# Optimization experiments

Hardware: AMD Instinct MI355X
Metric: run time of the kernel (lower is better)

The kernel has to match this reference:

```python
import jax, jax.numpy as jnp
import numpy as np

BS, T, E, H, CU = 8, 1024, 512, 8, 6
HD = E // H
W_SCALE = 0.05  # keep pre-softmax logits in a sane range


def setup_inputs() -> dict:
    key = jax.random.key(0)
    ks = jax.random.split(key, 9)
    return {
        "x": jax.random.normal(ks[0], (BS, T, E), jnp.float32),
        "u": jax.random.normal(ks[1], (BS, CU, T, T), jnp.float32),
        "umask": jnp.zeros((BS, T, T, 1), jnp.bool_),
        "wq": jax.random.normal(ks[2], (E, E), jnp.float32) * W_SCALE,
        "wk": jax.random.normal(ks[3], (E, E), jnp.float32) * W_SCALE,
        "wv": jax.random.normal(ks[4], (E, E), jnp.float32) * W_SCALE,
        "wo": jax.random.normal(ks[5], (E, E), jnp.float32) * W_SCALE,
        "bo": jnp.zeros((E,), jnp.float32),
        "wu": jax.random.normal(ks[6], (H, CU), jnp.float32) * W_SCALE,
        "bu": jnp.zeros((H,), jnp.float32),
    }


def reference(x, u, umask, wq, wk, wv, wo, bo, wu, bu):
    bs, t, e = x.shape
    h, hd = H, HD
    scaling = hd ** (-0.5)

    # linear projections (torch Linear: y = x @ W^T), split heads -> [b, h, t, hd]
    def proj(w):
        return jnp.einsum('bte,fe->btf', x, w).reshape(bs, t, h, hd).transpose(0, 2, 1, 3)

    Q, K, V = proj(wq), proj(wk), proj(wv)

    # NOTE: faithful to source, which DIVIDES by head_dim**-0.5
    scores = jnp.einsum('bhqd,bhkd->bhqk', Q, K) / scaling

    # 1x1 conv bias projection: [b, cu, t, t] -> [b, h, t, t]
    ubias = jnp.einsum('bcij,hc->bhij', u, wu) + bu[None, :, None, None]
    # umask: [b, t, t, 1] -> swap dims 1 and 3 -> [b, 1, t, t]
    mask_t = jnp.transpose(umask, (0, 3, 2, 1))
    ubias = jnp.where(mask_t, -jnp.inf, ubias)
    scores = scores + ubias

    attn = jax.nn.softmax(scores, axis=-1)
    # dropout p=0.0 -> identity
    ctx = jnp.einsum('bhqk,bhkd->bqhd', attn, V).reshape(bs, t, e)
    out = jnp.einsum('bte,fe->btf', ctx, wo) + bo
    return (out, attn)
```

## Files before the change

### kernel.cpp

```cpp
#include <hip/hip_runtime.h>
#include <cmath>

#define BSZ 8
#define TT  1024
#define EE  512
#define HH  8
#define CUc 6
#define HDD 64

typedef __bf16 bf16;
typedef __attribute__((ext_vector_type(4))) float f32x4;
typedef __attribute__((ext_vector_type(8))) float f32x8;
typedef __attribute__((ext_vector_type(4))) bf16  bf16x4;
typedef __attribute__((ext_vector_type(8))) bf16  bf16x8;

static __device__ __forceinline__ f32x4 mfma16(bf16x8 a, bf16x8 b, f32x4 c) {
    return __builtin_amdgcn_mfma_f32_16x16x32_bf16(a, b, c, 0, 0, 0);
}
static __device__ __forceinline__ void glds16(const bf16* g, bf16* l) {
    __builtin_amdgcn_global_load_lds((const __attribute__((address_space(1))) void*)g,
                                     (__attribute__((address_space(3))) void*)l, 16, 0, 0);
}

__global__ __launch_bounds__(256) void k_split_all(
    const float* __restrict__ wq, const float* __restrict__ wk,
    const float* __restrict__ wv, const float* __restrict__ wo,
    bf16* __restrict__ wqh, bf16* __restrict__ wql,
    bf16* __restrict__ wkh, bf16* __restrict__ wkl,
    bf16* __restrict__ wvh, bf16* __restrict__ woh)
{
    const float* src; bf16* hi; bf16* lo;
    switch (blockIdx.y) {
        case 0: src = wq; hi = wqh; lo = wql;     break;
        case 1: src = wk; hi = wkh; lo = wkl;     break;
        case 2: src = wv; hi = wvh; lo = nullptr; break;
        default: src = wo; hi = woh; lo = nullptr; break;
    }
    const int i = (blockIdx.x * 256 + threadIdx.x) * 8;
    f32x8 v = *(const f32x8*)(src + i);
    bf16x8 h8, l8;
#pragma unroll
    for (int k = 0; k < 8; ++k) {
        bf16 h = (bf16)v[k];
        h8[k] = h;
        l8[k] = (bf16)(v[k] - (float)h);
    }
    *(bf16x8*)(hi + i) = h8;
    if (lo) *(bf16x8*)(lo + i) = l8;
}

__global__ __launch_bounds__(256) void k_proj2(
    const float* __restrict__ x,
    const bf16* __restrict__ wqh, const bf16* __restrict__ wql,
    const bf16* __restrict__ wkh, const bf16* __restrict__ wkl,
    const bf16* __restrict__ wvh,
    bf16* __restrict__ Qh, bf16* __restrict__ Ql,
    bf16* __restrict__ Kh, bf16* __restrict__ Kl,
    bf16* __restrict__ Vt)
{
    const int rb = blockIdx.x;
    const int cb = blockIdx.y;
    const int wid = threadIdx.x >> 6;
    const int l   = threadIdx.x & 63;
    const int lg = l >> 4, lr = l & 15;
    const int row = rb * 64 + wid * 16 + lr;

    f32x4 aq[4], ak[4], av[4];
#pragma unroll
    for (int c = 0; c < 4; ++c) {
        aq[c] = f32x4{0.f,0.f,0.f,0.f}; ak[c] = f32x4{0.f,0.f,0.f,0.f}; av[c] = f32x4{0.f,0.f,0.f,0.f};
    }

    for (int ks = 0; ks < 16; ++ks) {
        const int e0 = ks * 32 + lg * 8;
        f32x8 xv = *(const f32x8*)(x + (size_t)row * EE + e0);
        bf16x8 xh, xl;
#pragma unroll
        for (int i = 0; i < 8; ++i) {
            bf16 h = (bf16)xv[i];
            xh[i] = h;
            xl[i] = (bf16)(xv[i] - (float)h);
        }
#pragma unroll
        for (int c = 0; c < 4; ++c) {
            const int f = cb * 64 + c * 16 + lr;
            const size_t wo = (size_t)f * EE + e0;
            bf16x8 qh = *(const bf16x8*)(wqh + wo);
            bf16x8 ql = *(const bf16x8*)(wql + wo);
            bf16x8 kh = *(const bf16x8*)(wkh + wo);
            bf16x8 kl = *(const bf16x8*)(wkl + wo);
            bf16x8 vh = *(const bf16x8*)(wvh + wo);
            aq[c] = mfma16(xh, qh, aq[c]); aq[c] = mfma16(xh, ql, aq[c]); aq[c] = mfma16(xl, qh, aq[c]);
            ak[c] = mfma16(xh, kh, ak[c]); ak[c] = mfma16(xh, kl, ak[c]); ak[c] = mfma16(xl, kh, ak[c]);
            av[c] = mfma16(xh, vh, av[c]);
        }
    }

#pragma unroll
    for (int c = 0; c < 4; ++c)
#pragma unroll
        for (int r = 0; r < 4; ++r) {
            const int orow = rb * 64 + wid * 16 + lg * 4 + r;
            const int b = orow >> 10, t = orow & 1023;
            const int f = cb * 64 + c * 16 + lr;
            const int h = f >> 6, d = f & 63;
            const size_t idx = ((size_t)(b * HH + h) * TT + t) * HDD + d;
            float vq = aq[c][r];
            bf16 qhi = (bf16)vq; Qh[idx] = qhi; Ql[idx] = (bf16)(vq - (float)qhi);
            float vk = ak[c][r];
            bf16 khi = (bf16)vk; Kh[idx] = khi; Kl[idx] = (bf16)(vk - (float)khi);
            Vt[(((size_t)(b * HH + h) * HDD + d) * TT) + t] = (bf16)av[c][r];
        }
}

__global__ __launch_bounds__(256) void k_ubias2(
    const float* __restrict__ u, const unsigned char* __restrict__ umask,
    const float* __restrict__ wu, const float* __restrict__ bu,
    float* __restrict__ A)
{
    __shared__ __align__(16) unsigned char msk[64][64];
    const int b  = blockIdx.z;
    const int i0 = blockIdx.y * 64;
    const int j0 = blockIdx.x * 64;
    const int t  = threadIdx.x;

    {
        const int jj  = t >> 2;
        const int seg = (t & 3) * 16;
        *(uint4*)(&msk[jj][seg]) =
            *(const uint4*)(umask + ((size_t)b * TT + (j0 + jj)) * TT + i0 + seg);
    }
    float wuv[HH][CUc], buv[HH];
#pragma unroll
    for (int h = 0; h < HH; ++h) {
        buv[h] = bu[h];
#pragma unroll
        for (int c = 0; c < CUc; ++c) wuv[h][c] = wu[h * CUc + c];
    }
    __syncthreads();

    const int j = j0 + (t & 63);
    for (int ii = (t >> 6); ii < 64; ii += 4) {
        const int i = i0 + ii;
        float uv[CUc];
#pragma unroll
        for (int c = 0; c < CUc; ++c)
            uv[c] = u[(((size_t)b * CUc + c) * TT + i) * TT + j];
        const bool mk = msk[t & 63][ii] != 0;
#pragma unroll
        for (int h = 0; h < HH; ++h) {
            float v = buv[h];
#pragma unroll
            for (int c = 0; c < CUc; ++c) v += uv[c] * wuv[h][c];
            if (mk) v = -INFINITY;
            bf16* ub = (bf16*)(A + ((size_t)(b * HH + h) * TT + (i & ~15)) * TT);
            ub[(i & 15) * TT + j] = (bf16)v;
        }
    }
}

__global__ __launch_bounds__(512, 1) void kf10(
    const bf16* __restrict__ Qh, const bf16* __restrict__ Ql,
    const bf16* __restrict__ Kh, const bf16* __restrict__ Kl,
    const bf16* __restrict__ Vt,
    float* __restrict__ A, bf16* __restrict__ ctx)
{
    const int g  = blockIdx.x;
    const int b  = g & 7;
    const int hh = g >> 6;
    const int ib = (g >> 3) & 7;
    const int bh = b * HH + hh;
    const int i0 = ib * 128;
    const int w  = threadIdx.x >> 6;
    const int l  = threadIdx.x & 63;
    const int lg = l >> 4, lr = l & 15;
    const int i16c = ib * 8 + w;
    const int iw   = i0 + w * 16;

    __shared__ __align__(16) bf16 KHL[2][8192];
    __shared__ __align__(16) bf16 KLL[2][8192];
    __shared__ __align__(16) bf16 VL [2][8192];
    __shared__ __align__(16) bf16 P  [8][2048];
    __shared__ float mh[8][16][12];

    const bf16* KhG = Kh + (size_t)bh * TT * HDD;
    const bf16* KlG = Kl + (size_t)bh * TT * HDD;
    const bf16* VtG = Vt + (size_t)bh * HDD * TT;
    bf16* Aw = (bf16*)(A + ((size_t)bh * TT + i16c * 16) * TT);

    const bf16* qph = Qh + ((size_t)bh * TT + iw) * HDD;
    const bf16* qpl = Ql + ((size_t)bh * TT + iw) * HDD;
    bf16x8 qh0 = *(const bf16x8*)(qph + lr * HDD + lg * 8);
    bf16x8 qh1 = *(const bf16x8*)(qph + lr * HDD + 32 + lg * 8);
    bf16x8 ql0 = *(const bf16x8*)(qpl + lr * HDD + lg * 8);
    bf16x8 ql1 = *(const bf16x8*)(qpl + lr * HDD + 32 + lg * 8);

    auto stage = [&](int buf, int t) {
        const int j0 = t * 128;
#pragma unroll
        for (int k = 0; k < 6; ++k) {
            const int gu = w * 6 + k;
            if (gu < 16) {
                const int u = gu;
                const int jr = u * 8 + (l >> 3), s = l & 7;
                glds16(KhG + (size_t)(j0 + jr) * HDD + ((s ^ (jr & 7)) * 8),
                       &KHL[buf][u * 512]);
            } else if (gu < 32) {
                const int u = gu - 16;
                const int jr = u * 8 + (l >> 3), s = l & 7;
                glds16(KlG + (size_t)(j0 + jr) * HDD + ((s ^ (jr & 7)) * 8),
                       &KLL[buf][u * 512]);
            } else {
                const int u = gu - 32;
                const int d = u * 4 + (l >> 4), s = l & 15;
                const int q = (s & 8) | ((s ^ (d & 7)) & 7);
                glds16(VtG + (size_t)d * TT + j0 + q * 8,
                       &VL[buf][u * 512]);
            }
        }
    };

    float m_run[4], s_run[4];
    f32x4 cacc[4];
#pragma unroll
    for (int r = 0; r < 4; ++r) { m_run[r] = -INFINITY; s_run[r] = 0.f; }
#pragma unroll
    for (int dt = 0; dt < 4; ++dt) cacc[dt] = f32x4{0.f,0.f,0.f,0.f};

    stage(0, 0);
    __syncthreads();

    for (int t = 0; t < 8; ++t) {
        const int buf = t & 1;

        bf16x8 ubr[4];
#pragma unroll
        for (int q = 0; q < 4; ++q) {
            const int r = q * 4 + (l >> 4), s = l & 15;
            ubr[q] = *(const bf16x8*)(Aw + (size_t)r * TT + t * 128 + s * 8);
        }
        if (t < 7) stage(buf ^ 1, t + 1);

        f32x4 s8[8];
#pragma unroll
        for (int jt2 = 0; jt2 < 8; ++jt2) {
            const int jr = jt2 * 16 + lr;
            const int x7 = jr & 7;
            bf16x8 kh0 = *(const bf16x8*)&KHL[buf][jr * 64 + ((lg       ^ x7) * 8)];
            bf16x8 kh1 = *(const bf16x8*)&KHL[buf][jr * 64 + (((lg + 4) ^ x7) * 8)];
            bf16x8 kl0 = *(const bf16x8*)&KLL[buf][jr * 64 + ((lg       ^ x7) * 8)];
            bf16x8 kl1 = *(const bf16x8*)&KLL[buf][jr * 64 + (((lg + 4) ^ x7) * 8)];
            f32x4 acc = f32x4{0.f,0.f,0.f,0.f};
            acc = mfma16(qh0, kh0, acc); acc = mfma16(qh1, kh1, acc);
            acc = mfma16(qh0, kl0, acc); acc = mfma16(qh1, kl1, acc);
            acc = mfma16(ql0, kh0, acc); acc = mfma16(ql1, kh1, acc);
            s8[jt2] = acc;
        }

#pragma unroll
        for (int q = 0; q < 4; ++q) {
            const int r = q * 4 + (l >> 4), s = l & 15;
            const int slot = (s & 8) | ((s ^ (r & 7)) & 7);
            *(bf16x8*)&P[w][r * 128 + slot * 8] = ubr[q];
        }
#pragma unroll
        for (int jt2 = 0; jt2 < 8; ++jt2)
#pragma unroll
            for (int r = 0; r < 4; ++r) {
                const int row = lg * 4 + r, col = jt2 * 16 + lr;
                const int sg = col >> 3;
                const int slot = (sg & 8) | ((sg ^ (row & 7)) & 7);
                s8[jt2][r] = s8[jt2][r] * 8.0f + (float)P[w][row * 128 + slot * 8 + (col & 7)];
            }

        float tm[4];
#pragma unroll
        for (int r = 0; r < 4; ++r) {
            float mm = s8[0][r];
#pragma unroll
            for (int jt2 = 1; jt2 < 8; ++jt2) mm = fmaxf(mm, s8[jt2][r]);
            tm[r] = mm;
        }
#pragma unroll
        for (int off = 1; off < 16; off <<= 1)
#pragma unroll
            for (int r = 0; r < 4; ++r) tm[r] = fmaxf(tm[r], __shfl_xor(tm[r], off));
        float mnew[4], mexp[4], e[4];
#pragma unroll
        for (int r = 0; r < 4; ++r) {
            mnew[r] = fmaxf(m_run[r], tm[r]);
            mexp[r] = (mnew[r] == -INFINITY) ? 0.f : mnew[r];
            e[r]    = (m_run[r] == -INFINITY) ? 0.f : __expf(m_run[r] - mexp[r]);
            m_run[r] = mnew[r];
        }
#pragma unroll
        for (int dt = 0; dt < 4; ++dt)
#pragma unroll
            for (int r = 0; r < 4; ++r) cacc[dt][r] *= e[r];

        float psum[4] = {0.f, 0.f, 0.f, 0.f};
#pragma unroll
        for (int jt2 = 0; jt2 < 8; ++jt2)
#pragma unroll
            for (int r = 0; r < 4; ++r) {
                const float p = __expf(s8[jt2][r] - mexp[r]);
                psum[r] += p;
                const int row = lg * 4 + r, col = jt2 * 16 + lr;
                const int sg = col >> 3;
                const int slot = (sg & 8) | ((sg ^ (row & 7)) & 7);
                P[w][row * 128 + slot * 8 + (col & 7)] = (bf16)p;
            }
#pragma unroll
        for (int off = 1; off < 16; off <<= 1)
#pragma unroll
            for (int r = 0; r < 4; ++r) psum[r] += __shfl_xor(psum[r], off);
#pragma unroll
        for (int r = 0; r < 4; ++r) s_run[r] = s_run[r] * e[r] + psum[r];
        if (lr == 0)
#pragma unroll
            for (int r = 0; r < 4; ++r) mh[w][lg * 4 + r][t] = mnew[r];

#pragma unroll
        for (int q = 0; q < 4; ++q) {
            const int r = q * 4 + (l >> 4), s = l & 15;
            const int slot = (s & 8) | ((s ^ (r & 7)) & 7);
            bf16x8 pv = *(const bf16x8*)&P[w][r * 128 + slot * 8];
            *(bf16x8*)(Aw + (size_t)r * 2048 + 1024 + t * 128 + s * 8) = pv;
        }

#pragma unroll
        for (int ks = 0; ks < 4; ++ks) {
            const int sg = ks * 4 + lg;
            const int ps = (sg & 8) | ((sg ^ (lr & 7)) & 7);
            bf16x8 a = *(const bf16x8*)&P[w][lr * 128 + ps * 8];
#pragma unroll
            for (int dt = 0; dt < 4; ++dt) {
                const int d = dt * 16 + lr;
                const int vs = (sg & 8) | ((sg ^ (d & 7)) & 7);
                bf16x8 bv = *(const bf16x8*)&VL[buf][d * 128 + vs * 8];
                cacc[dt] = mfma16(a, bv, cacc[dt]);
            }
        }
        __syncthreads();
    }

    if (lr == 0)
#pragma unroll
        for (int r = 0; r < 4; ++r) mh[w][lg * 4 + r][8] = s_run[r];

    float invS[4], mfin[4];
#pragma unroll
    for (int q = 0; q < 4; ++q) {
        const int r = q * 4 + (l >> 4);
        mfin[q] = mh[w][r][7];
        invS[q] = 1.0f / mh[w][r][8];
    }
    float* Af = A + ((size_t)bh * TT + i16c * 16) * TT;
#pragma unroll
    for (int t = 0; t < 8; ++t) {
        bf16x8 pv[4];
        float fac[4];
#pragma unroll
        for (int q = 0; q < 4; ++q) {
            const int r = q * 4 + (l >> 4), s = l & 15;
            pv[q] = *(const bf16x8*)(Aw + (size_t)r * 2048 + 1024 + t * 128 + s * 8);
            fac[q] = __expf(mh[w][r][t] - mfin[q]) * invS[q];
        }
        asm volatile("s_waitcnt vmcnt(0)" ::: "memory");
#pragma unroll
        for (int q = 0; q < 4; ++q) {
            const int r = q * 4 + (l >> 4), s = l & 15;
            f32x4 o0, o1;
#pragma unroll
            for (int ee = 0; ee < 4; ++ee) {
                o0[ee] = (float)pv[q][ee]     * fac[q];
                o1[ee] = (float)pv[q][4 + ee] * fac[q];
            }
            *(f32x4*)(Af + (size_t)r * TT + t * 128 + s * 8)     = o0;
            *(f32x4*)(Af + (size_t)r * TT + t * 128 + s * 8 + 4) = o1;
        }
    }

#pragma unroll
    for (int r = 0; r < 4; ++r) {
        const float is = 1.0f / s_run[r];
        const int row = iw + lg * 4 + r;
#pragma unroll
        for (int dt = 0; dt < 4; ++dt)
            ctx[((size_t)b * TT + row) * EE + hh * HDD + dt * 16 + lr] = (bf16)(cacc[dt][r] * is);
    }
}

__global__ __launch_bounds__(256) void k_out2(
    const bf16* __restrict__ ctx, const bf16* __restrict__ woh,
    const float* __restrict__ bo, float* __restrict__ out)
{
    const int rb = blockIdx.x;
    const int cb = blockIdx.y;
    const int wid = threadIdx.x >> 6;
    const int l = threadIdx.x & 63;
    const int lg = l >> 4, lr = l & 15;
    const int row = rb * 64 + wid * 16 + lr;

    f32x4 acc[4];
#pragma unroll
    for (int c = 0; c < 4; ++c) acc[c] = f32x4{0.f,0.f,0.f,0.f};

    for (int ks = 0; ks < 16; ++ks) {
        const int e0 = ks * 32 + lg * 8;
        bf16x8 af = *(const bf16x8*)(ctx + (size_t)row * EE + e0);
#pragma unroll
        for (int c = 0; c < 4; ++c) {
            const int f = cb * 64 + c * 16 + lr;
            bf16x8 wf = *(const bf16x8*)(woh + (size_t)f * EE + e0);
            acc[c] = mfma16(af, wf, acc[c]);
        }
    }
#pragma unroll
    for (int c = 0; c < 4; ++c) {
        const int f = cb * 64 + c * 16 + lr;
        const float bov = bo[f];
#pragma unroll
        for (int r = 0; r < 4; ++r) {
            const int orow = rb * 64 + wid * 16 + lg * 4 + r;
            out[(size_t)orow * EE + f] = acc[c][r] + bov;
        }
    }
}

extern "C" void kernel_launch(void* const* d_in, const int* in_sizes, int n_in,
                              void* d_out, int out_size, void* d_ws, size_t ws_size,
                              hipStream_t stream)
{
    (void)in_sizes; (void)n_in; (void)out_size; (void)ws_size;
    const float* x  = (const float*)d_in[0];
    const float* u  = (const float*)d_in[1];
    const unsigned char* umask = (const unsigned char*)d_in[2];
    const float* wq = (const float*)d_in[3];
    const float* wk = (const float*)d_in[4];
    const float* wv = (const float*)d_in[5];
    const float* wo = (const float*)d_in[6];
    const float* bo = (const float*)d_in[7];
    const float* wu = (const float*)d_in[8];
    const float* bu = (const float*)d_in[9];

    float* out = (float*)d_out;
    float* A   = out + (size_t)BSZ * TT * EE;

    const size_t qs  = (size_t)BSZ * HH * TT * HDD;
    const size_t wsz = (size_t)EE * EE;
    bf16* Qh  = (bf16*)d_ws;
    bf16* Ql  = Qh + qs;
    bf16* Kh  = Ql + qs;
    bf16* Kl  = Kh + qs;
    bf16* Vt  = Kl + qs;
    bf16* ctx = Vt + qs;
    bf16* wqh = ctx + qs;
    bf16* wql = wqh + wsz;
    bf16* wkh = wql + wsz;
    bf16* wkl = wkh + wsz;
    bf16* wvh = wkl + wsz;
    bf16* woh = wvh + wsz;

    k_split_all<<<dim3(128, 4), 256, 0, stream>>>(wq, wk, wv, wo,
                                                  wqh, wql, wkh, wkl, wvh, woh);
    k_proj2 <<<dim3(128, 8), 256, 0, stream>>>(x, wqh, wql, wkh, wkl, wvh, Qh, Ql, Kh, Kl, Vt);
    k_ubias2<<<dim3(16, 16, 8), 256, 0, stream>>>(u, umask, wu, bu, A);
    kf10    <<<512, 512, 0, stream>>>(Qh, Ql, Kh, Kl, Vt, A, ctx);
    k_out2  <<<dim3(128, 8), 256, 0, stream>>>(ctx, woh, bo, out);
}
```

Baseline: 446.0 us.

## Prefetch ubias tiles a step ahead and double-buffer the attention rescale pass

The bias tile for the next key block is now loaded from global memory at the end of each iteration. The full __syncthreads is replaced by a raw s_barrier with a partial vmcnt wait, so those loads and the async LDS staging stay in flight across the barrier. The final rescale pass, which reads the stored bf16 probabilities and writes fp32 attention, now uses two register buffers so loads for chunk t+1 overlap the stores for chunk t, and the ctx write is moved ahead of it. The aim is to hide global-memory latency in the main loop and the epilogue. The manual vmcnt counting is fragile: if the outstanding-load count is wrong, the barrier may not wait for the staged data.

```diff
diff --git a/kernel.cpp b/kernel.cpp
--- a/kernel.cpp
+++ b/kernel.cpp
@@ -159,7 +159,7 @@
     }
 }
 
-__global__ __launch_bounds__(512, 1) void kf10(
+__global__ __launch_bounds__(512, 1) void kf11(
     const bf16* __restrict__ Qh, const bf16* __restrict__ Ql,
     const bf16* __restrict__ Kh, const bf16* __restrict__ Kl,
     const bf16* __restrict__ Vt,
@@ -228,17 +228,16 @@
     for (int dt = 0; dt < 4; ++dt) cacc[dt] = f32x4{0.f,0.f,0.f,0.f};
 
     stage(0, 0);
+    bf16x8 ubr[4];
+#pragma unroll
+    for (int q = 0; q < 4; ++q) {
+        const int r = q * 4 + (l >> 4), s = l & 15;
+        ubr[q] = *(const bf16x8*)(Aw + (size_t)r * TT + s * 8);
+    }
     __syncthreads();
 
     for (int t = 0; t < 8; ++t) {
         const int buf = t & 1;
-
-        bf16x8 ubr[4];
-#pragma unroll
-        for (int q = 0; q < 4; ++q) {
-            const int r = q * 4 + (l >> 4), s = l & 15;
-            ubr[q] = *(const bf16x8*)(Aw + (size_t)r * TT + t * 128 + s * 8);
-        }
         if (t < 7) stage(buf ^ 1, t + 1);
 
         f32x4 s8[8];
@@ -341,12 +340,36 @@
                 cacc[dt] = mfma16(a, bv, cacc[dt]);
             }
         }
-        __syncthreads();
+
+        if (t < 7) {
+#pragma unroll
+            for (int q = 0; q < 4; ++q) {
+                const int r = q * 4 + (l >> 4), s = l & 15;
+                ubr[q] = *(const bf16x8*)(Aw + (size_t)r * TT + (t + 1) * 128 + s * 8);
+            }
+            __builtin_amdgcn_sched_barrier(0);
+            asm volatile("s_waitcnt vmcnt(8)" ::: "memory");
+            __builtin_amdgcn_s_barrier();
+            __builtin_amdgcn_sched_barrier(0);
+        }
     }
 
     if (lr == 0)
 #pragma unroll
         for (int r = 0; r < 4; ++r) mh[w][lg * 4 + r][8] = s_run[r];
+
+#pragma unroll
+    for (int r = 0; r < 4; ++r) {
+        const float is = 1.0f / s_run[r];
+        const int row = iw + lg * 4 + r;
+#pragma unroll
+        for (int dt = 0; dt < 4; ++dt)
+            ctx[((size_t)b * TT + row) * EE + hh * HDD + dt * 16 + lr] = (bf16)(cacc[dt][r] * is);
+    }
+
+    __builtin_amdgcn_sched_barrier(0);
+    asm volatile("s_waitcnt vmcnt(0)" ::: "memory");
+    __builtin_amdgcn_sched_barrier(0);
 
     float invS[4], mfin[4];
 #pragma unroll
@@ -356,39 +379,42 @@
         invS[q] = 1.0f / mh[w][r][8];
     }
     float* Af = A + ((size_t)bh * TT + i16c * 16) * TT;
-#pragma unroll
-    for (int t = 0; t < 8; ++t) {
-        bf16x8 pv[4];
-        float fac[4];
-#pragma unroll
-        for (int q = 0; q < 4; ++q) {
-            const int r = q * 4 + (l >> 4), s = l & 15;
-            pv[q] = *(const bf16x8*)(Aw + (size_t)r * 2048 + 1024 + t * 128 + s * 8);
-            fac[q] = __expf(mh[w][r][t] - mfin[q]) * invS[q];
-        }
-        asm volatile("s_waitcnt vmcnt(0)" ::: "memory");
-#pragma unroll
-        for (int q = 0; q < 4; ++q) {
-            const int r = q * 4 + (l >> 4), s = l & 15;
-            f32x4 o0, o1;
-#pragma unroll
-            for (int ee = 0; ee < 4; ++ee) {
-                o0[ee] = (float)pv[q][ee]     * fac[q];
-                o1[ee] = (float)pv[q][4 + ee] * fac[q];
-            }
-            *(f32x4*)(Af + (size_t)r * TT + t * 128 + s * 8)     = o0;
-            *(f32x4*)(Af + (size_t)r * TT + t * 128 + s * 8 + 4) = o1;
-        }
-    }
-
-#pragma unroll
-    for (int r = 0; r < 4; ++r) {
-        const float is = 1.0f / s_run[r];
-        const int row = iw + lg * 4 + r;
-#pragma unroll
-        for (int dt = 0; dt < 4; ++dt)
-            ctx[((size_t)b * TT + row) * EE + hh * HDD + dt * 16 + lr] = (bf16)(cacc[dt][r] * is);
-    }
+
+#define LOADP(ARR, T) {                                                         \
+    _Pragma("unroll")                                                           \
+    for (int q = 0; q < 4; ++q) {                                               \
+        const int r = q * 4 + (l >> 4), s = l & 15;                             \
+        ARR[q] = *(const bf16x8*)(Aw + (size_t)r * 2048 + 1024 + (T) * 128 + s * 8); \
+    }                                                                           \
+  }
+#define PROCP(ARR, T) {                                                         \
+    _Pragma("unroll")                                                           \
+    for (int q = 0; q < 4; ++q) {                                               \
+        const int r = q * 4 + (l >> 4), s = l & 15;                             \
+        const float fac = __expf(mh[w][r][T] - mfin[q]) * invS[q];              \
+        f32x4 o0, o1;                                                           \
+        _Pragma("unroll")                                                       \
+        for (int ee = 0; ee < 4; ++ee) {                                        \
+            o0[ee] = (float)ARR[q][ee]     * fac;                               \
+            o1[ee] = (float)ARR[q][4 + ee] * fac;                               \
+        }                                                                       \
+        *(f32x4*)(Af + (size_t)r * TT + (T) * 128 + s * 8)     = o0;            \
+        *(f32x4*)(Af + (size_t)r * TT + (T) * 128 + s * 8 + 4) = o1;            \
+    }                                                                           \
+  }
+
+    bf16x8 pvA[4], pvB[4];
+    LOADP(pvA, 0); LOADP(pvB, 1);
+    PROCP(pvA, 0); LOADP(pvA, 2);
+    PROCP(pvB, 1); LOADP(pvB, 3);
+    PROCP(pvA, 2); LOADP(pvA, 4);
+    PROCP(pvB, 3); LOADP(pvB, 5);
+    PROCP(pvA, 4); LOADP(pvA, 6);
+    PROCP(pvB, 5); LOADP(pvB, 7);
+    PROCP(pvA, 6);
+    PROCP(pvB, 7);
+#undef LOADP
+#undef PROCP
 }
 
 __global__ __launch_bounds__(256) void k_out2(
@@ -466,6 +492,6 @@
                                                   wqh, wql, wkh, wkl, wvh, woh);
     k_proj2 <<<dim3(128, 8), 256, 0, stream>>>(x, wqh, wql, wkh, wkl, wvh, Qh, Ql, Kh, Kl, Vt);
     k_ubias2<<<dim3(16, 16, 8), 256, 0, stream>>>(u, umask, wu, bu, A);
-    kf10    <<<512, 512, 0, stream>>>(Qh, Ql, Kh, Kl, Vt, A, ctx);
+    kf11    <<<512, 512, 0, stream>>>(Qh, Ql, Kh, Kl, Vt, A, ctx);
     k_out2  <<<dim3(128, 8), 256, 0, stream>>>(ctx, woh, bo, out);
 }
```

After: 448.6 us. Within noise of the previous version (+0.6%).

## Recompute QK scores in a second pass instead of spilling unnormalized P

Applied to the files above, without the earlier changes.

The attention kernel previously wrote unnormalized bf16 probabilities to the attention buffer each tile, then reread them and rescaled by per-tile max factors in an epilogue. Now the first pass only computes the running max/sum and context, and a second pass recomputes QK^T with K-only staging, adds the bias again, and writes the final normalized probabilities directly. The ubias kernel writes into the upper half of each row pair so the bias survives the first pass, and barriers are replaced with explicit vmcnt waits plus s_barrier for prefetching the bias. This trades extra MFMA work and K reloads for removing one round trip of the P scratch through global memory.

```diff
diff --git a/kernel.cpp b/kernel.cpp
--- a/kernel.cpp
+++ b/kernel.cpp
@@ -154,12 +154,12 @@
             for (int c = 0; c < CUc; ++c) v += uv[c] * wuv[h][c];
             if (mk) v = -INFINITY;
             bf16* ub = (bf16*)(A + ((size_t)(b * HH + h) * TT + (i & ~15)) * TT);
-            ub[(i & 15) * TT + j] = (bf16)v;
-        }
-    }
-}
-
-__global__ __launch_bounds__(512, 1) void kf10(
+            ub[(i & 15) * 2048 + 1024 + j] = (bf16)v;
+        }
+    }
+}
+
+__global__ __launch_bounds__(512, 1) void kf12(
     const bf16* __restrict__ Qh, const bf16* __restrict__ Ql,
     const bf16* __restrict__ Kh, const bf16* __restrict__ Kl,
     const bf16* __restrict__ Vt,
@@ -181,7 +181,7 @@
     __shared__ __align__(16) bf16 KLL[2][8192];
     __shared__ __align__(16) bf16 VL [2][8192];
     __shared__ __align__(16) bf16 P  [8][2048];
-    __shared__ float mh[8][16][12];
+    __shared__ float sM[8][16], sS[8][16];
 
     const bf16* KhG = Kh + (size_t)bh * TT * HDD;
     const bf16* KlG = Kl + (size_t)bh * TT * HDD;
@@ -201,21 +201,32 @@
         for (int k = 0; k < 6; ++k) {
             const int gu = w * 6 + k;
             if (gu < 16) {
-                const int u = gu;
-                const int jr = u * 8 + (l >> 3), s = l & 7;
-                glds16(KhG + (size_t)(j0 + jr) * HDD + ((s ^ (jr & 7)) * 8),
-                       &KHL[buf][u * 512]);
+                const int jr = gu * 8 + (l >> 3), s = l & 7;
+                glds16(KhG + (size_t)(j0 + jr) * HDD + ((s ^ (jr & 7)) * 8), &KHL[buf][gu * 512]);
             } else if (gu < 32) {
                 const int u = gu - 16;
                 const int jr = u * 8 + (l >> 3), s = l & 7;
-                glds16(KlG + (size_t)(j0 + jr) * HDD + ((s ^ (jr & 7)) * 8),
-                       &KLL[buf][u * 512]);
+                glds16(KlG + (size_t)(j0 + jr) * HDD + ((s ^ (jr & 7)) * 8), &KLL[buf][u * 512]);
             } else {
                 const int u = gu - 32;
                 const int d = u * 4 + (l >> 4), s = l & 15;
                 const int q = (s & 8) | ((s ^ (d & 7)) & 7);
-                glds16(VtG + (size_t)d * TT + j0 + q * 8,
-                       &VL[buf][u * 512]);
+                glds16(VtG + (size_t)d * TT + j0 + q * 8, &VL[buf][u * 512]);
+            }
+        }
+    };
+    auto stageK = [&](int buf, int t) {
+        const int j0 = t * 128;
+#pragma unroll
+        for (int k = 0; k < 4; ++k) {
+            const int gu = w * 4 + k;
+            if (gu < 16) {
+                const int jr = gu * 8 + (l >> 3), s = l & 7;
+                glds16(KhG + (size_t)(j0 + jr) * HDD + ((s ^ (jr & 7)) * 8), &KHL[buf][gu * 512]);
+            } else {
+                const int u = gu - 16;
+                const int jr = u * 8 + (l >> 3), s = l & 7;
+                glds16(KlG + (size_t)(j0 + jr) * HDD + ((s ^ (jr & 7)) * 8), &KLL[buf][u * 512]);
             }
         }
     };
@@ -227,18 +238,18 @@
 #pragma unroll
     for (int dt = 0; dt < 4; ++dt) cacc[dt] = f32x4{0.f,0.f,0.f,0.f};
 
+    bf16x8 ubr[4];
+
     stage(0, 0);
+#pragma unroll
+    for (int q = 0; q < 4; ++q) {
+        const int r = q * 4 + (l >> 4), s = l & 15;
+        ubr[q] = *(const bf16x8*)(Aw + (size_t)r * 2048 + 1024 + s * 8);
+    }
     __syncthreads();
 
     for (int t = 0; t < 8; ++t) {
         const int buf = t & 1;
-
-        bf16x8 ubr[4];
-#pragma unroll
-        for (int q = 0; q < 4; ++q) {
-            const int r = q * 4 + (l >> 4), s = l & 15;
-            ubr[q] = *(const bf16x8*)(Aw + (size_t)r * TT + t * 128 + s * 8);
-        }
         if (t < 7) stage(buf ^ 1, t + 1);
 
         f32x4 s8[8];
@@ -316,17 +327,6 @@
             for (int r = 0; r < 4; ++r) psum[r] += __shfl_xor(psum[r], off);
 #pragma unroll
         for (int r = 0; r < 4; ++r) s_run[r] = s_run[r] * e[r] + psum[r];
-        if (lr == 0)
-#pragma unroll
-            for (int r = 0; r < 4; ++r) mh[w][lg * 4 + r][t] = mnew[r];
-
-#pragma unroll
-        for (int q = 0; q < 4; ++q) {
-            const int r = q * 4 + (l >> 4), s = l & 15;
-            const int slot = (s & 8) | ((s ^ (r & 7)) & 7);
-            bf16x8 pv = *(const bf16x8*)&P[w][r * 128 + slot * 8];
-            *(bf16x8*)(Aw + (size_t)r * 2048 + 1024 + t * 128 + s * 8) = pv;
-        }
 
 #pragma unroll
         for (int ks = 0; ks < 4; ++ks) {
@@ -341,45 +341,23 @@
                 cacc[dt] = mfma16(a, bv, cacc[dt]);
             }
         }
-        __syncthreads();
+
+        if (t < 7) {
+#pragma unroll
+            for (int q = 0; q < 4; ++q) {
+                const int r = q * 4 + (l >> 4), s = l & 15;
+                ubr[q] = *(const bf16x8*)(Aw + (size_t)r * 2048 + 1024 + (t + 1) * 128 + s * 8);
+            }
+            __builtin_amdgcn_sched_barrier(0);
+            asm volatile("s_waitcnt vmcnt(4)" ::: "memory");
+            __builtin_amdgcn_s_barrier();
+            __builtin_amdgcn_sched_barrier(0);
+        }
     }
 
     if (lr == 0)
 #pragma unroll
-        for (int r = 0; r < 4; ++r) mh[w][lg * 4 + r][8] = s_run[r];
-
-    float invS[4], mfin[4];
-#pragma unroll
-    for (int q = 0; q < 4; ++q) {
-        const int r = q * 4 + (l >> 4);
-        mfin[q] = mh[w][r][7];
-        invS[q] = 1.0f / mh[w][r][8];
-    }
-    float* Af = A + ((size_t)bh * TT + i16c * 16) * TT;
-#pragma unroll
-    for (int t = 0; t < 8; ++t) {
-        bf16x8 pv[4];
-        float fac[4];
-#pragma unroll
-        for (int q = 0; q < 4; ++q) {
-            const int r = q * 4 + (l >> 4), s = l & 15;
-            pv[q] = *(const bf16x8*)(Aw + (size_t)r * 2048 + 1024 + t * 128 + s * 8);
-            fac[q] = __expf(mh[w][r][t] - mfin[q]) * invS[q];
-        }
-        asm volatile("s_waitcnt vmcnt(0)" ::: "memory");
-#pragma unroll
-        for (int q = 0; q < 4; ++q) {
-            const int r = q * 4 + (l >> 4), s = l & 15;
-            f32x4 o0, o1;
-#pragma unroll
-            for (int ee = 0; ee < 4; ++ee) {
-                o0[ee] = (float)pv[q][ee]     * fac[q];
-                o1[ee] = (float)pv[q][4 + ee] * fac[q];
-            }
-            *(f32x4*)(Af + (size_t)r * TT + t * 128 + s * 8)     = o0;
-            *(f32x4*)(Af + (size_t)r * TT + t * 128 + s * 8 + 4) = o1;
-        }
-    }
+        for (int r = 0; r < 4; ++r) { sM[w][lg * 4 + r] = m_run[r]; sS[w][lg * 4 + r] = s_run[r]; }
 
 #pragma unroll
     for (int r = 0; r < 4; ++r) {
@@ -388,6 +366,101 @@
 #pragma unroll
         for (int dt = 0; dt < 4; ++dt)
             ctx[((size_t)b * TT + row) * EE + hh * HDD + dt * 16 + lr] = (bf16)(cacc[dt][r] * is);
+    }
+    __syncthreads();
+
+    float invSk[8];
+#pragma unroll
+    for (int k = 0; k < 8; ++k) invSk[k] = 1.0f / sS[w][(l >> 5) + 2 * k];
+    float mfc[4];
+#pragma unroll
+    for (int r = 0; r < 4; ++r) {
+        const float m = sM[w][lg * 4 + r];
+        mfc[r] = (m == -INFINITY) ? 0.f : m;
+    }
+    float* Af = A + ((size_t)bh * TT + i16c * 16) * TT;
+
+    stageK(0, 0);
+#pragma unroll
+    for (int q = 0; q < 4; ++q) {
+        const int r = q * 4 + (l >> 4), s = l & 15;
+        ubr[q] = *(const bf16x8*)(Aw + (size_t)r * 2048 + 1024 + s * 8);
+    }
+    __builtin_amdgcn_sched_barrier(0);
+    asm volatile("s_waitcnt vmcnt(4)" ::: "memory");
+    __builtin_amdgcn_s_barrier();
+    __builtin_amdgcn_sched_barrier(0);
+
+    for (int t = 0; t < 8; ++t) {
+        const int buf = t & 1;
+        if (t < 7) stageK(buf ^ 1, t + 1);
+
+        f32x4 s8[8];
+#pragma unroll
+        for (int jt2 = 0; jt2 < 8; ++jt2) {
+            const int jr = jt2 * 16 + lr;
+            const int x7 = jr & 7;
+            bf16x8 kh0 = *(const bf16x8*)&KHL[buf][jr * 64 + ((lg       ^ x7) * 8)];
+            bf16x8 kh1 = *(const bf16x8*)&KHL[buf][jr * 64 + (((lg + 4) ^ x7) * 8)];
+            bf16x8 kl0 = *(const bf16x8*)&KLL[buf][jr * 64 + ((lg       ^ x7) * 8)];
+            bf16x8 kl1 = *(const bf16x8*)&KLL[buf][jr * 64 + (((lg + 4) ^ x7) * 8)];
+            f32x4 acc = f32x4{0.f,0.f,0.f,0.f};
+            acc = mfma16(qh0, kh0, acc); acc = mfma16(qh1, kh1, acc);
+            acc = mfma16(qh0, kl0, acc); acc = mfma16(qh1, kl1, acc);
+            acc = mfma16(ql0, kh0, acc); acc = mfma16(ql1, kh1, acc);
+            s8[jt2] = acc;
+        }
+
+#pragma unroll
+        for (int q = 0; q < 4; ++q) {
+            const int r = q * 4 + (l >> 4), s = l & 15;
+            const int slot = (s & 8) | ((s ^ (r & 7)) & 7);
+            *(bf16x8*)&P[w][r * 128 + slot * 8] = ubr[q];
+        }
+#pragma unroll
+        for (int jt2 = 0; jt2 < 8; ++jt2)
+#pragma unroll
+            for (int r = 0; r < 4; ++r) {
+                const int row = lg * 4 + r, col = jt2 * 16 + lr;
+                const int sg = col >> 3;
+                const int slot = (sg & 8) | ((sg ^ (row & 7)) & 7);
+                s8[jt2][r] = s8[jt2][r] * 8.0f + (float)P[w][row * 128 + slot * 8 + (col & 7)];
+            }
+
+#pragma unroll
+        for (int jt2 = 0; jt2 < 8; ++jt2)
+#pragma unroll
+            for (int r = 0; r < 4; ++r) {
+                const int row = lg * 4 + r, col = jt2 * 16 + lr;
+                const int sg = col >> 3;
+                const int slot = (sg & 8) | ((sg ^ (row & 7)) & 7);
+                P[w][row * 128 + slot * 8 + (col & 7)] = (bf16)__expf(s8[jt2][r] - mfc[r]);
+            }
+
+#pragma unroll
+        for (int k = 0; k < 8; ++k) {
+            const int pr = (l >> 5) + 2 * k;
+            const int c0 = (l & 31) * 4;
+            const int sg = c0 >> 3;
+            const int slot = (sg & 8) | ((sg ^ (pr & 7)) & 7);
+            bf16x4 pv = *(const bf16x4*)&P[w][pr * 128 + slot * 8 + (c0 & 7)];
+            f32x4 o;
+#pragma unroll
+            for (int ee = 0; ee < 4; ++ee) o[ee] = (float)pv[ee] * invSk[k];
+            *(f32x4*)(Af + (size_t)pr * TT + t * 128 + c0) = o;
+        }
+
+        if (t < 7) {
+#pragma unroll
+            for (int q = 0; q < 4; ++q) {
+                const int r = q * 4 + (l >> 4), s = l & 15;
+                ubr[q] = *(const bf16x8*)(Aw + (size_t)r * 2048 + 1024 + (t + 1) * 128 + s * 8);
+            }
+            __builtin_amdgcn_sched_barrier(0);
+            asm volatile("s_waitcnt vmcnt(12)" ::: "memory");
+            __builtin_amdgcn_s_barrier();
+            __builtin_amdgcn_sched_barrier(0);
+        }
     }
 }
 
@@ -466,6 +539,6 @@
                                                   wqh, wql, wkh, wkl, wvh, woh);
     k_proj2 <<<dim3(128, 8), 256, 0, stream>>>(x, wqh, wql, wkh, wkl, wvh, Qh, Ql, Kh, Kl, Vt);
     k_ubias2<<<dim3(16, 16, 8), 256, 0, stream>>>(u, umask, wu, bu, A);
-    kf10    <<<512, 512, 0, stream>>>(Qh, Ql, Kh, Kl, Vt, A, ctx);
+    kf12    <<<512, 512, 0, stream>>>(Qh, Ql, Kh, Kl, Vt, A, ctx);
     k_out2  <<<dim3(128, 8), 256, 0, stream>>>(ctx, woh, bo, out);
 }
```

Result: no change. 443.4 us (-0.6%).
